# Kernel tuning notes

Hardware: AMD Instinct MI355X
Metric: run time of the kernel (lower is better)

Reference implementation:

```python
import jax, jax.numpy as jnp
import numpy as np


def setup_inputs() -> dict:
    key = jax.random.key(0)
    ks = jax.random.split(key, 6)
    B, d, S = 256, 512, 196  # batch, hidden dim, spatial locations (14x14)
    return {
        "memory_state": jax.random.normal(ks[0], (B, d), dtype=jnp.float32),
        "ctrl_state": jax.random.normal(ks[1], (B, d), dtype=jnp.float32),
        "kb_proj": jax.random.normal(ks[2], (B, d, S), dtype=jnp.float32),
        "W_concat": jax.random.normal(ks[3], (d, d), dtype=jnp.float32) * (1.0 / np.sqrt(d)),
        "b_concat": jax.random.normal(ks[4], (d,), dtype=jnp.float32) * 0.01,
        "w_attn": jax.random.normal(ks[5], (d,), dtype=jnp.float32) * (1.0 / np.sqrt(d)),
    }


def reference(memory_state, ctrl_state, kb_proj, W_concat, b_concat, w_attn):
    # I_elements: [B, S, d] -- elementwise gating of knowledge base by memory
    I_t = memory_state[:, :, None] * kb_proj           # [B, d, S]
    I_t = jnp.transpose(I_t, (0, 2, 1))                # [B, S, d]
    # concat_layer (torch Linear: x @ W^T + b) + residual with kb_proj
    concat = jnp.einsum('bsd,ed->bse', I_t, W_concat) + b_concat
    concat = concat + jnp.transpose(kb_proj, (0, 2, 1))  # [B, S, d]
    # attention logits: (concat * ctrl) @ w_attn -> [B, S]
    rai = jnp.einsum('bsd,d->bs', concat * ctrl_state[:, None, :], w_attn)
    rvi = jax.nn.softmax(rai, axis=1)                  # [B, S]
    # attention-weighted sum over spatial locations -> [B, d]
    read_vector = jnp.einsum('bs,bds->bd', rvi, kb_proj)
    return read_vector
```

## Files before the change

### kernel.cpp

```cpp
#include <hip/hip_runtime.h>
#include <math.h>

#define B 256
#define D 512
#define S 196
#define SQ 49
#define NCH 8
#define NINST 49

__device__ __forceinline__ void stage1k(const float* __restrict__ g,
                                        float* lds_base, int lane) {
    __builtin_amdgcn_global_load_lds(
        (const __attribute__((address_space(1))) void*)(g + 4 * lane),
        (__attribute__((address_space(3))) void*)lds_base,
        16, 0, 0);
}

__global__ __launch_bounds__(256) void k_gemm(const float* __restrict__ ctrl,
                                              const float* __restrict__ w_attn,
                                              const float* __restrict__ W,
                                              float* __restrict__ gpart) {
    __shared__ float u_s[64][8];
    const int ce = blockIdx.x >> 5;
    const int b0 = (blockIdx.x & 31) * 8;
    const int t = threadIdx.x;
#pragma unroll
    for (int k = t; k < 512; k += 256) {
        const int j = k & 7, el = k >> 3;
        const int e = ce * 64 + el;
        u_s[el][j] = ctrl[(b0 + j) * D + e] * w_attn[e];
    }
    __syncthreads();
    float a0[8], a1[8];
#pragma unroll
    for (int j = 0; j < 8; ++j) { a0[j] = 0.f; a1[j] = 0.f; }
    for (int e0 = 0; e0 < 64; e0 += 4) {
        float w0[4], w1[4];
#pragma unroll
        for (int i = 0; i < 4; ++i) {
            const int e = ce * 64 + e0 + i;
            w0[i] = W[e * D + t];
            w1[i] = W[e * D + t + 256];
        }
#pragma unroll
        for (int i = 0; i < 4; ++i) {
            const float4 ua = *(const float4*)&u_s[e0 + i][0];
            const float4 ub = *(const float4*)&u_s[e0 + i][4];
            a0[0] += ua.x * w0[i]; a0[1] += ua.y * w0[i];
            a0[2] += ua.z * w0[i]; a0[3] += ua.w * w0[i];
            a0[4] += ub.x * w0[i]; a0[5] += ub.y * w0[i];
            a0[6] += ub.z * w0[i]; a0[7] += ub.w * w0[i];
            a1[0] += ua.x * w1[i]; a1[1] += ua.y * w1[i];
            a1[2] += ua.z * w1[i]; a1[3] += ua.w * w1[i];
            a1[4] += ub.x * w1[i]; a1[5] += ub.y * w1[i];
            a1[6] += ub.z * w1[i]; a1[7] += ub.w * w1[i];
        }
    }
#pragma unroll
    for (int j = 0; j < 8; ++j) {
        gpart[((size_t)(b0 + j) * NCH + ce) * D + t]       = a0[j];
        gpart[((size_t)(b0 + j) * NCH + ce) * D + t + 256] = a1[j];
    }
}

__global__ __launch_bounds__(256) void k_logits(const float* __restrict__ kb,
                                                const float* __restrict__ gpart,
                                                const float* __restrict__ mem,
                                                const float* __restrict__ ctrl,
                                                const float* __restrict__ w_attn,
                                                float* __restrict__ rai_part) {
    __shared__ float kb_s[64 * S];
    __shared__ float p_s[64];
    __shared__ float part[4][S];
    const int bid = blockIdx.x;
    const int b = bid >> 3, c = bid & 7;
    const int t = threadIdx.x;
    const int w = t >> 6, l = t & 63;
    const float* base = kb + (size_t)b * D * S + (size_t)c * 64 * S;

    for (int inst = w; inst < NINST; inst += 4)
        stage1k(base + inst * 256, &kb_s[inst * 256], l);

    if (t < 64) {
        const int d = c * 64 + t;
        float s = 0.f;
#pragma unroll
        for (int ce = 0; ce < NCH; ++ce)
            s += gpart[((size_t)b * NCH + ce) * D + d];
        p_s[t] = mem[b * D + d] * s + ctrl[b * D + d] * w_attn[d];
    }
    __syncthreads();

    if (l < SQ) {
        float4 acc = {0.f, 0.f, 0.f, 0.f};
#pragma unroll
        for (int i = 0; i < 16; ++i) {
            const int r = w * 16 + i;
            const float4 v = *(const float4*)&kb_s[r * S + 4 * l];
            const float pv = p_s[r];
            acc.x += pv * v.x; acc.y += pv * v.y;
            acc.z += pv * v.z; acc.w += pv * v.w;
        }
        *(float4*)&part[w][4 * l] = acc;
    }
    __syncthreads();
    if (t < S)
        rai_part[(size_t)bid * S + t] = (part[0][t] + part[1][t]) + (part[2][t] + part[3][t]);
}

__global__ __launch_bounds__(256) void k_wsum(const float* __restrict__ kb,
                                              const float* __restrict__ rai_part,
                                              float* __restrict__ out) {
    __shared__ float kb_s[64 * S];
    __shared__ float rvi_s[S];
    __shared__ float redm[4], reds[4];
    const int bid = blockIdx.x;
    const int b = bid >> 3, c = bid & 7;
    const int t = threadIdx.x;
    const int w = t >> 6, l = t & 63;
    const float* base = kb + (size_t)b * D * S + (size_t)c * 64 * S;

    for (int inst = w; inst < NINST; inst += 4)
        stage1k(base + inst * 256, &kb_s[inst * 256], l);

    float rai = -INFINITY;
    if (t < S) {
        float v = 0.f;
#pragma unroll
        for (int k = 0; k < NCH; ++k)
            v += rai_part[((size_t)b * NCH + k) * S + t];
        rai = v;
    }
    float m = rai;
#pragma unroll
    for (int o = 1; o < 64; o <<= 1) m = fmaxf(m, __shfl_xor(m, o, 64));
    if (l == 0) redm[w] = m;
    __syncthreads();
    m = fmaxf(fmaxf(redm[0], redm[1]), fmaxf(redm[2], redm[3]));
    float ex = (t < S) ? __expf(rai - m) : 0.f;
    float sm = ex;
#pragma unroll
    for (int o = 1; o < 64; o <<= 1) sm += __shfl_xor(sm, o, 64);
    if (l == 0) reds[w] = sm;
    __syncthreads();
    const float li = (reds[0] + reds[1]) + (reds[2] + reds[3]);
    if (t < S) rvi_s[t] = ex / li;
    __syncthreads();

    float4 rv = {0.f, 0.f, 0.f, 0.f};
    if (l < SQ) rv = *(const float4*)&rvi_s[4 * l];
#pragma unroll
    for (int i = 0; i < 16; ++i) {
        const int r = w * 16 + i;
        float a = 0.f;
        if (l < SQ) {
            const float4 v = *(const float4*)&kb_s[r * S + 4 * l];
            a = rv.x * v.x + rv.y * v.y + rv.z * v.z + rv.w * v.w;
        }
#pragma unroll
        for (int o = 1; o < 64; o <<= 1) a += __shfl_xor(a, o, 64);
        if (l == 0) out[(size_t)b * D + c * 64 + r] = a;
    }
}

extern "C" void kernel_launch(void* const* d_in, const int* in_sizes, int n_in,
                              void* d_out, int out_size, void* d_ws, size_t ws_size,
                              hipStream_t stream) {
    const float* mem  = (const float*)d_in[0];
    const float* ctrl = (const float*)d_in[1];
    const float* kb   = (const float*)d_in[2];
    const float* W    = (const float*)d_in[3];
    const float* wat  = (const float*)d_in[5];
    float* out = (float*)d_out;

    float* gpart    = (float*)d_ws;
    float* rai_part = gpart + (size_t)B * NCH * D;

    k_gemm  <<<256,     256, 0, stream>>>(ctrl, wat, W, gpart);
    k_logits<<<B * NCH, 256, 0, stream>>>(kb, gpart, mem, ctrl, wat, rai_part);
    k_wsum  <<<B * NCH, 256, 0, stream>>>(kb, rai_part, out);
}
```

Measured before the change: 198.0 us.

## Fuse gemm, logits and weighted-sum into one cooperative kernel with grid sync

Replaces the three-kernel pipeline with one cooperative kernel of 512 blocks that runs four rounds. Each round loads a 64-row kb chunk into LDS once and uses it for both the logits and the final weighted sum, so kb is no longer read from HBM twice. A grid-wide sync between the two uses lets the per-batch softmax see all partial logits. The W·(ctrl*w_attn) matvec is now recomputed for each chunk inside the block rather than done once in a separate GEMM kernel. The change trades extra redundant compute, W traffic through L2 and four grid barriers for half the kb traffic and two fewer launches.

```diff
diff --git a/kernel.cpp b/kernel.cpp
--- a/kernel.cpp
+++ b/kernel.cpp
@@ -1,11 +1,15 @@
 #include <hip/hip_runtime.h>
+#include <hip/hip_cooperative_groups.h>
 #include <math.h>
+
+namespace cg = cooperative_groups;
 
 #define B 256
 #define D 512
 #define S 196
 #define SQ 49
-#define NCH 8
+#define GRID 512
+#define ROUNDS 4
 #define NINST 49
 
 __device__ __forceinline__ void stage1k(const float* __restrict__ g,
@@ -16,150 +20,123 @@
         16, 0, 0);
 }
 
-__global__ __launch_bounds__(256) void k_gemm(const float* __restrict__ ctrl,
+__global__ __launch_bounds__(256) void k_coop(const float* __restrict__ mem,
+                                              const float* __restrict__ ctrl,
+                                              const float* __restrict__ W,
                                               const float* __restrict__ w_attn,
-                                              const float* __restrict__ W,
-                                              float* __restrict__ gpart) {
-    __shared__ float u_s[64][8];
-    const int ce = blockIdx.x >> 5;
-    const int b0 = (blockIdx.x & 31) * 8;
-    const int t = threadIdx.x;
-#pragma unroll
-    for (int k = t; k < 512; k += 256) {
-        const int j = k & 7, el = k >> 3;
-        const int e = ce * 64 + el;
-        u_s[el][j] = ctrl[(b0 + j) * D + e] * w_attn[e];
-    }
-    __syncthreads();
-    float a0[8], a1[8];
-#pragma unroll
-    for (int j = 0; j < 8; ++j) { a0[j] = 0.f; a1[j] = 0.f; }
-    for (int e0 = 0; e0 < 64; e0 += 4) {
-        float w0[4], w1[4];
-#pragma unroll
-        for (int i = 0; i < 4; ++i) {
-            const int e = ce * 64 + e0 + i;
-            w0[i] = W[e * D + t];
-            w1[i] = W[e * D + t + 256];
-        }
-#pragma unroll
-        for (int i = 0; i < 4; ++i) {
-            const float4 ua = *(const float4*)&u_s[e0 + i][0];
-            const float4 ub = *(const float4*)&u_s[e0 + i][4];
-            a0[0] += ua.x * w0[i]; a0[1] += ua.y * w0[i];
-            a0[2] += ua.z * w0[i]; a0[3] += ua.w * w0[i];
-            a0[4] += ub.x * w0[i]; a0[5] += ub.y * w0[i];
-            a0[6] += ub.z * w0[i]; a0[7] += ub.w * w0[i];
-            a1[0] += ua.x * w1[i]; a1[1] += ua.y * w1[i];
-            a1[2] += ua.z * w1[i]; a1[3] += ua.w * w1[i];
-            a1[4] += ub.x * w1[i]; a1[5] += ub.y * w1[i];
-            a1[6] += ub.z * w1[i]; a1[7] += ub.w * w1[i];
-        }
-    }
-#pragma unroll
-    for (int j = 0; j < 8; ++j) {
-        gpart[((size_t)(b0 + j) * NCH + ce) * D + t]       = a0[j];
-        gpart[((size_t)(b0 + j) * NCH + ce) * D + t + 256] = a1[j];
-    }
-}
-
-__global__ __launch_bounds__(256) void k_logits(const float* __restrict__ kb,
-                                                const float* __restrict__ gpart,
-                                                const float* __restrict__ mem,
-                                                const float* __restrict__ ctrl,
-                                                const float* __restrict__ w_attn,
-                                                float* __restrict__ rai_part) {
+                                              const float* __restrict__ kb,
+                                              float* __restrict__ rai_all,
+                                              float* __restrict__ out) {
     __shared__ float kb_s[64 * S];
     __shared__ float p_s[64];
     __shared__ float part[4][S];
-    const int bid = blockIdx.x;
-    const int b = bid >> 3, c = bid & 7;
+    __shared__ float rvi_s[S];
+    __shared__ float pred[4][64];
+    __shared__ float redm[4], reds[4];
+    cg::grid_group grid = cg::this_grid();
+
+    const int g = blockIdx.x;
     const int t = threadIdx.x;
     const int w = t >> 6, l = t & 63;
-    const float* base = kb + (size_t)b * D * S + (size_t)c * 64 * S;
 
-    for (int inst = w; inst < NINST; inst += 4)
-        stage1k(base + inst * 256, &kb_s[inst * 256], l);
+    {
+        const float* base0 = kb + (size_t)g * 64 * S;
+        for (int inst = w; inst < NINST; inst += 4)
+            stage1k(base0 + inst * 256, &kb_s[inst * 256], l);
+    }
 
-    if (t < 64) {
-        const int d = c * 64 + t;
-        float s = 0.f;
+#pragma unroll 1
+    for (int r = 0; r < ROUNDS; ++r) {
+        const int chunk = g + GRID * r;
+        const int b = chunk >> 3, c = chunk & 7;
+
+        {
+            float acc = 0.f;
+            for (int i = 0; i < 128; i += 8) {
+                float wv[8], uv[8];
 #pragma unroll
-        for (int ce = 0; ce < NCH; ++ce)
-            s += gpart[((size_t)b * NCH + ce) * D + d];
-        p_s[t] = mem[b * D + d] * s + ctrl[b * D + d] * w_attn[d];
-    }
-    __syncthreads();
+                for (int j = 0; j < 8; ++j) {
+                    const int e = w * 128 + i + j;
+                    wv[j] = W[e * D + c * 64 + l];
+                    uv[j] = ctrl[b * D + e] * w_attn[e];
+                }
+#pragma unroll
+                for (int j = 0; j < 8; ++j) acc += uv[j] * wv[j];
+            }
+            pred[w][l] = acc;
+        }
+        __syncthreads();
+        if (t < 64) {
+            const int d = c * 64 + t;
+            const float s = (pred[0][t] + pred[1][t]) + (pred[2][t] + pred[3][t]);
+            p_s[t] = mem[b * D + d] * s + ctrl[b * D + d] * w_attn[d];
+        }
+        __syncthreads();
 
-    if (l < SQ) {
-        float4 acc = {0.f, 0.f, 0.f, 0.f};
+        if (l < SQ) {
+            float4 acc = {0.f, 0.f, 0.f, 0.f};
+#pragma unroll
+            for (int i = 0; i < 16; ++i) {
+                const int row = w * 16 + i;
+                const float4 v = *(const float4*)&kb_s[row * S + 4 * l];
+                const float pv = p_s[row];
+                acc.x += pv * v.x; acc.y += pv * v.y;
+                acc.z += pv * v.z; acc.w += pv * v.w;
+            }
+            *(float4*)&part[w][4 * l] = acc;
+        }
+        __syncthreads();
+        if (t < S)
+            rai_all[(size_t)chunk * S + t] =
+                (part[0][t] + part[1][t]) + (part[2][t] + part[3][t]);
+
+        grid.sync();
+
+        float rai = -INFINITY;
+        if (t < S) {
+            float v = 0.f;
+#pragma unroll
+            for (int k = 0; k < 8; ++k)
+                v += rai_all[((size_t)b * 8 + k) * S + t];
+            rai = v;
+        }
+        float m = rai;
+#pragma unroll
+        for (int o = 1; o < 64; o <<= 1) m = fmaxf(m, __shfl_xor(m, o, 64));
+        if (l == 0) redm[w] = m;
+        __syncthreads();
+        m = fmaxf(fmaxf(redm[0], redm[1]), fmaxf(redm[2], redm[3]));
+        float ex = (t < S) ? __expf(rai - m) : 0.f;
+        float sm = ex;
+#pragma unroll
+        for (int o = 1; o < 64; o <<= 1) sm += __shfl_xor(sm, o, 64);
+        if (l == 0) reds[w] = sm;
+        __syncthreads();
+        const float li = (reds[0] + reds[1]) + (reds[2] + reds[3]);
+        if (t < S) rvi_s[t] = ex / li;
+        __syncthreads();
+
+        float4 rv = {0.f, 0.f, 0.f, 0.f};
+        if (l < SQ) rv = *(const float4*)&rvi_s[4 * l];
 #pragma unroll
         for (int i = 0; i < 16; ++i) {
-            const int r = w * 16 + i;
-            const float4 v = *(const float4*)&kb_s[r * S + 4 * l];
-            const float pv = p_s[r];
-            acc.x += pv * v.x; acc.y += pv * v.y;
-            acc.z += pv * v.z; acc.w += pv * v.w;
+            const int row = w * 16 + i;
+            float a = 0.f;
+            if (l < SQ) {
+                const float4 v = *(const float4*)&kb_s[row * S + 4 * l];
+                a = rv.x * v.x + rv.y * v.y + rv.z * v.z + rv.w * v.w;
+            }
+#pragma unroll
+            for (int o = 1; o < 64; o <<= 1) a += __shfl_xor(a, o, 64);
+            if (l == 0) out[(size_t)b * D + c * 64 + row] = a;
         }
-        *(float4*)&part[w][4 * l] = acc;
-    }
-    __syncthreads();
-    if (t < S)
-        rai_part[(size_t)bid * S + t] = (part[0][t] + part[1][t]) + (part[2][t] + part[3][t]);
-}
+        __syncthreads();
 
-__global__ __launch_bounds__(256) void k_wsum(const float* __restrict__ kb,
-                                              const float* __restrict__ rai_part,
-                                              float* __restrict__ out) {
-    __shared__ float kb_s[64 * S];
-    __shared__ float rvi_s[S];
-    __shared__ float redm[4], reds[4];
-    const int bid = blockIdx.x;
-    const int b = bid >> 3, c = bid & 7;
-    const int t = threadIdx.x;
-    const int w = t >> 6, l = t & 63;
-    const float* base = kb + (size_t)b * D * S + (size_t)c * 64 * S;
-
-    for (int inst = w; inst < NINST; inst += 4)
-        stage1k(base + inst * 256, &kb_s[inst * 256], l);
-
-    float rai = -INFINITY;
-    if (t < S) {
-        float v = 0.f;
-#pragma unroll
-        for (int k = 0; k < NCH; ++k)
-            v += rai_part[((size_t)b * NCH + k) * S + t];
-        rai = v;
-    }
-    float m = rai;
-#pragma unroll
-    for (int o = 1; o < 64; o <<= 1) m = fmaxf(m, __shfl_xor(m, o, 64));
-    if (l == 0) redm[w] = m;
-    __syncthreads();
-    m = fmaxf(fmaxf(redm[0], redm[1]), fmaxf(redm[2], redm[3]));
-    float ex = (t < S) ? __expf(rai - m) : 0.f;
-    float sm = ex;
-#pragma unroll
-    for (int o = 1; o < 64; o <<= 1) sm += __shfl_xor(sm, o, 64);
-    if (l == 0) reds[w] = sm;
-    __syncthreads();
-    const float li = (reds[0] + reds[1]) + (reds[2] + reds[3]);
-    if (t < S) rvi_s[t] = ex / li;
-    __syncthreads();
-
-    float4 rv = {0.f, 0.f, 0.f, 0.f};
-    if (l < SQ) rv = *(const float4*)&rvi_s[4 * l];
-#pragma unroll
-    for (int i = 0; i < 16; ++i) {
-        const int r = w * 16 + i;
-        float a = 0.f;
-        if (l < SQ) {
-            const float4 v = *(const float4*)&kb_s[r * S + 4 * l];
-            a = rv.x * v.x + rv.y * v.y + rv.z * v.z + rv.w * v.w;
+        if (r + 1 < ROUNDS) {
+            const float* basen = kb + (size_t)(chunk + GRID) * 64 * S;
+            for (int inst = w; inst < NINST; inst += 4)
+                stage1k(basen + inst * 256, &kb_s[inst * 256], l);
         }
-#pragma unroll
-        for (int o = 1; o < 64; o <<= 1) a += __shfl_xor(a, o, 64);
-        if (l == 0) out[(size_t)b * D + c * 64 + r] = a;
     }
 }
 
@@ -172,11 +149,10 @@
     const float* W    = (const float*)d_in[3];
     const float* wat  = (const float*)d_in[5];
     float* out = (float*)d_out;
+    float* rai_all = (float*)d_ws;
 
-    float* gpart    = (float*)d_ws;
-    float* rai_part = gpart + (size_t)B * NCH * D;
-
-    k_gemm  <<<256,     256, 0, stream>>>(ctrl, wat, W, gpart);
-    k_logits<<<B * NCH, 256, 0, stream>>>(kb, gpart, mem, ctrl, wat, rai_part);
-    k_wsum  <<<B * NCH, 256, 0, stream>>>(kb, rai_part, out);
+    void* args[] = {(void*)&mem, (void*)&ctrl, (void*)&W, (void*)&wat,
+                    (void*)&kb, (void*)&rai_all, (void*)&out};
+    hipLaunchCooperativeKernel((const void*)k_coop, dim3(GRID), dim3(256),
+                               args, 0, stream);
 }
```

Measured after the change: 456.2 us. +130.4%, slower.
